# Kernel optimization log

Hardware: AMD Instinct MI355X
Metric: run time of the kernel (lower is better)

## Reference

```python
import jax, jax.numpy as jnp
import numpy as np

E, H, FF = 1024, 16, 4096
HD = E // H
B, S = 4, 2048


def _ln(x, g, b, eps=1e-5):
    m = jnp.mean(x, axis=-1, keepdims=True)
    v = jnp.mean((x - m) ** 2, axis=-1, keepdims=True)
    return (x - m) / jnp.sqrt(v + eps) * g + b


def setup_inputs() -> dict:
    k = jax.random.key(0)
    ks = jax.random.split(k, 12)
    sd = 0.02
    return {
        "value": jax.random.normal(ks[0], (B, S, E), jnp.float32),
        "key": jax.random.normal(ks[1], (B, S, E), jnp.float32),
        "query": jax.random.normal(ks[2], (B, S, E), jnp.float32),
        "mask": jnp.ones((B, 1, 1, S), jnp.int32),
        "Wv": sd * jax.random.normal(ks[3], (E, E), jnp.float32),
        "Wk": sd * jax.random.normal(ks[4], (E, E), jnp.float32),
        "Wq": sd * jax.random.normal(ks[5], (E, E), jnp.float32),
        "Wo": sd * jax.random.normal(ks[6], (E, E), jnp.float32),
        "bo": jnp.zeros((E,), jnp.float32),
        "ln1_g": jnp.ones((E,), jnp.float32), "ln1_b": jnp.zeros((E,), jnp.float32),
        "ln2_g": jnp.ones((E,), jnp.float32), "ln2_b": jnp.zeros((E,), jnp.float32),
        "lnf_g": jnp.ones((E,), jnp.float32), "lnf_b": jnp.zeros((E,), jnp.float32),
        "W1": sd * jax.random.normal(ks[7], (E, FF), jnp.float32),
        "b1": jnp.zeros((FF,), jnp.float32),
        "W2": sd * jax.random.normal(ks[8], (FF, E), jnp.float32),
        "b2": jnp.zeros((E,), jnp.float32),
    }


def reference(value, key, query, mask, Wv, Wk, Wq, Wo, bo,
              ln1_g, ln1_b, ln2_g, ln2_b, lnf_g, lnf_b, W1, b1, W2, b2):
    N, Sq, Em = query.shape
    # pre-norms (value & key share prenorm2 params, as in the torch module)
    v = _ln(value, ln2_g, ln2_b)
    k = _ln(key, ln2_g, ln2_b)
    q = _ln(query, ln1_g, ln1_b)
    # QKV projections (no bias), split heads
    V = (v @ Wv).reshape(N, v.shape[1], H, HD)
    K = (k @ Wk).reshape(N, k.shape[1], H, HD)
    Q = (q @ Wq).reshape(N, Sq, H, HD)
    energy = jnp.einsum("nqhd,nkhd->nhqk", Q, K)  # [N,H,Sq,Sk]
    energy = jnp.where(mask == 0, jnp.float32(-1e20), energy)
    attn = jax.nn.softmax(energy / jnp.float32(HD ** 0.5), axis=-1)
    out = jnp.einsum("nhqk,nkhd->nqhd", attn, V).reshape(N, Sq, Em)
    out = out @ Wo + bo
    x = out + q  # residual (drop_path is identity in eval)
    f = _ln(x, lnf_g, lnf_b) @ W1 + b1
    f = jax.nn.gelu(f, approximate=False) @ W2 + b2
    return f + x
```

## Files before the change

### kernel.cpp

```cpp
#include <hip/hip_runtime.h>
#include <hip/hip_bf16.h>
#include <math.h>

typedef __bf16 bf16x8 __attribute__((ext_vector_type(8)));
typedef __bf16 bf16x4 __attribute__((ext_vector_type(4)));
typedef float f32x4 __attribute__((ext_vector_type(4)));
typedef float f32x2 __attribute__((ext_vector_type(2)));
typedef short s16x4 __attribute__((ext_vector_type(4)));

#define AS1 __attribute__((address_space(1)))
#define AS3 __attribute__((address_space(3)))

__device__ __forceinline__ void gll16(const __bf16* g, __bf16* l) {
    __builtin_amdgcn_global_load_lds((const AS1 unsigned int*)g,
                                     (AS3 unsigned int*)l, 16, 0, 0);
}

#if __has_builtin(__builtin_amdgcn_exp2f)
#define EXP2(x) __builtin_amdgcn_exp2f(x)
#else
#define EXP2(x) __expf((x) * 0.69314718055994530942f)
#endif

__device__ __forceinline__ f32x4 mfma16x16(bf16x4 a, bf16x4 b, f32x4 c) {
#if __has_builtin(__builtin_amdgcn_mfma_f32_16x16x16bf16_1k)
    union { bf16x4 h; s16x4 s; } ua, ub;
    ua.h = a; ub.h = b;
    return __builtin_amdgcn_mfma_f32_16x16x16bf16_1k(ua.s, ub.s, c, 0, 0, 0);
#else
    f32x4 d = c;
    asm volatile("v_mfma_f32_16x16x16_bf16 %0, %1, %2, %0"
                 : "+v"(d) : "v"(a), "v"(b));
    return d;
#endif
}

__global__ __launch_bounds__(256) void transpose_all(
    const float* __restrict__ Wq, const float* __restrict__ Wk,
    const float* __restrict__ Wv, const float* __restrict__ Wo,
    const float* __restrict__ W1, const float* __restrict__ W2,
    __bf16* __restrict__ Wqt, __bf16* __restrict__ Wkt,
    __bf16* __restrict__ Wvt, __bf16* __restrict__ Wot,
    __bf16* __restrict__ W1t, __bf16* __restrict__ W2t) {
    int g = blockIdx.x;
    const float* W; __bf16* Wt; int K, N, kt, nt;
    if (g < 4096) {
        int mi = g >> 10, loc = g & 1023;
        K = 1024; N = 1024; kt = loc >> 5; nt = loc & 31;
        W  = mi == 0 ? Wq  : mi == 1 ? Wk  : mi == 2 ? Wv  : Wo;
        Wt = mi == 0 ? Wqt : mi == 1 ? Wkt : mi == 2 ? Wvt : Wot;
    } else if (g < 8192) {
        int loc = g - 4096; W = W1; Wt = W1t;
        K = 1024; N = 4096; kt = loc >> 7; nt = loc & 127;
    } else {
        int loc = g - 8192; W = W2; Wt = W2t;
        K = 4096; N = 1024; kt = loc >> 5; nt = loc & 31;
    }
    int k0 = kt * 32, n0 = nt * 32;
    __shared__ float tile[32][33];
    int tx = threadIdx.x & 31, ty = threadIdx.x >> 5;
    #pragma unroll
    for (int j = ty; j < 32; j += 8)
        tile[j][tx] = W[(size_t)(k0 + j) * N + n0 + tx];
    __syncthreads();
    #pragma unroll
    for (int j = ty; j < 32; j += 8)
        Wt[(size_t)(n0 + j) * K + k0 + tx] = (__bf16)tile[tx][j];
}

__global__ __launch_bounds__(256) void ln3_kernel(
    const float* __restrict__ q, const float* __restrict__ k,
    const float* __restrict__ v,
    const float* __restrict__ g1, const float* __restrict__ b1,
    const float* __restrict__ g2, const float* __restrict__ b2,
    float* __restrict__ qln, __bf16* __restrict__ qbf,
    __bf16* __restrict__ kbf, __bf16* __restrict__ vbf) {
    const int E = 1024;
    int which = blockIdx.y;
    const float* x = which == 0 ? q : which == 1 ? k : v;
    const float* g = which == 0 ? g1 : g2;
    const float* bb = which == 0 ? b1 : b2;
    float* o32 = which == 0 ? qln : nullptr;
    __bf16* obf = which == 0 ? qbf : which == 1 ? kbf : vbf;

    size_t row = blockIdx.x;
    int t = threadIdx.x;
    float4 val = ((const float4*)(x + row * E))[t];
    float s  = val.x + val.y + val.z + val.w;
    float s2 = val.x * val.x + val.y * val.y + val.z * val.z + val.w * val.w;
    #pragma unroll
    for (int off = 32; off >= 1; off >>= 1) {
        s  += __shfl_down(s, off);
        s2 += __shfl_down(s2, off);
    }
    __shared__ float red[2][4];
    int wid = t >> 6, lane = t & 63;
    if (lane == 0) { red[0][wid] = s; red[1][wid] = s2; }
    __syncthreads();
    if (t == 0) {
        float S1 = red[0][0] + red[0][1] + red[0][2] + red[0][3];
        float S2 = red[1][0] + red[1][1] + red[1][2] + red[1][3];
        float mean = S1 / E;
        float var  = S2 / E - mean * mean;
        red[0][0] = mean;
        red[1][0] = 1.0f / sqrtf(var + 1e-5f);
    }
    __syncthreads();
    float mean = red[0][0], rstd = red[1][0];
    float4 gv = ((const float4*)g)[t];
    float4 bv = ((const float4*)bb)[t];
    float y0 = (val.x - mean) * rstd * gv.x + bv.x;
    float y1 = (val.y - mean) * rstd * gv.y + bv.y;
    float y2 = (val.z - mean) * rstd * gv.z + bv.z;
    float y3 = (val.w - mean) * rstd * gv.w + bv.w;
    if (o32) ((float4*)(o32 + row * E))[t] = make_float4(y0, y1, y2, y3);
    bf16x4 o;
    o[0] = (__bf16)y0; o[1] = (__bf16)y1; o[2] = (__bf16)y2; o[3] = (__bf16)y3;
    ((bf16x4*)(obf + row * E))[t] = o;
}

__global__ __launch_bounds__(256) void ln_kernel(const float* __restrict__ x,
                                                 const float* __restrict__ g,
                                                 const float* __restrict__ bb,
                                                 __bf16* __restrict__ outbf) {
    const int E = 1024;
    size_t row = blockIdx.x;
    int t = threadIdx.x;
    float4 v = ((const float4*)(x + row * E))[t];
    float s  = v.x + v.y + v.z + v.w;
    float s2 = v.x * v.x + v.y * v.y + v.z * v.z + v.w * v.w;
    #pragma unroll
    for (int off = 32; off >= 1; off >>= 1) {
        s  += __shfl_down(s, off);
        s2 += __shfl_down(s2, off);
    }
    __shared__ float red[2][4];
    int wid = t >> 6, lane = t & 63;
    if (lane == 0) { red[0][wid] = s; red[1][wid] = s2; }
    __syncthreads();
    if (t == 0) {
        float S1 = red[0][0] + red[0][1] + red[0][2] + red[0][3];
        float S2 = red[1][0] + red[1][1] + red[1][2] + red[1][3];
        float mean = S1 / E;
        float var  = S2 / E - mean * mean;
        red[0][0] = mean;
        red[1][0] = 1.0f / sqrtf(var + 1e-5f);
    }
    __syncthreads();
    float mean = red[0][0], rstd = red[1][0];
    float4 gv = ((const float4*)g)[t];
    float4 bv = ((const float4*)bb)[t];
    bf16x4 o;
    o[0] = (__bf16)((v.x - mean) * rstd * gv.x + bv.x);
    o[1] = (__bf16)((v.y - mean) * rstd * gv.y + bv.y);
    o[2] = (__bf16)((v.z - mean) * rstd * gv.z + bv.z);
    o[3] = (__bf16)((v.w - mean) * rstd * gv.w + bv.w);
    ((bf16x4*)(outbf + row * E))[t] = o;
}

template <int EPI>
__global__ __launch_bounds__(256) void gemm128(const __bf16* __restrict__ A,
                                               const __bf16* __restrict__ A2,
                                               const __bf16* __restrict__ Bt,
                                               const __bf16* __restrict__ Bt2,
                                               const float* __restrict__ bias,
                                               const float* __restrict__ resid,
                                               void* __restrict__ Cout,
                                               int M, int N, int K,
                                               int splitN, float scale) {
    __shared__ __bf16 As[128 * 64];
    __shared__ __bf16 Bs[128 * 64];
    int tid  = threadIdx.x;
    int lane = tid & 63, wid = tid >> 6;
    int quad = lane >> 4, l15 = lane & 15;
    int waveM = wid >> 1, waveN = wid & 1;

    int GX = N >> 7;
    int id = blockIdx.x;
    int x8 = id & 7, t = id >> 3;
    size_t rowBase = (size_t)((t / GX) * 8 + x8) * 128;
    size_t colBase = (size_t)(t % GX) * 128;

    const __bf16* Ap = A; const __bf16* Bp = Bt;
    size_t colLoc = colBase;
    float sc = scale;
    if ((int)colBase >= splitN) { Ap = A2; Bp = Bt2; colLoc = colBase - splitN; sc = 1.0f; }

    int lrow8  = lane >> 3;
    int lchunk = (lane & 7) ^ lrow8;
    const __bf16* Ag0 = Ap + (rowBase + wid * 32 + lrow8) * (size_t)K + lchunk * 8;
    const __bf16* Bg0 = Bp + (colLoc  + wid * 32 + lrow8) * (size_t)K + lchunk * 8;
    __bf16* AsB = &As[(wid * 32) * 64];
    __bf16* BsB = &Bs[(wid * 32) * 64];

    f32x4 acc[4][4] = {};
    int swz = l15 & 7;

    for (int kb = 0; kb < K; kb += 64) {
        __syncthreads();
        #pragma unroll
        for (int i = 0; i < 4; i++) {
            gll16(Ag0 + (size_t)i * 8 * K + kb, AsB + i * 512);
            gll16(Bg0 + (size_t)i * 8 * K + kb, BsB + i * 512);
        }
        __syncthreads();
        #pragma unroll
        for (int ks = 0; ks < 2; ks++) {
            int p = ((ks * 4 + quad) ^ swz) * 8;
            bf16x8 af[4], bfr[4];
            #pragma unroll
            for (int mi = 0; mi < 4; mi++)
                af[mi] = *(const bf16x8*)&As[(waveM * 64 + mi * 16 + l15) * 64 + p];
            #pragma unroll
            for (int ni = 0; ni < 4; ni++)
                bfr[ni] = *(const bf16x8*)&Bs[(waveN * 64 + ni * 16 + l15) * 64 + p];
            #pragma unroll
            for (int mi = 0; mi < 4; mi++)
                #pragma unroll
                for (int ni = 0; ni < 4; ni++)
                    acc[mi][ni] = __builtin_amdgcn_mfma_f32_16x16x32_bf16(
                        bfr[ni], af[mi], acc[mi][ni], 0, 0, 0);
        }
    }

    #pragma unroll
    for (int mi = 0; mi < 4; mi++)
    #pragma unroll
    for (int ni = 0; ni < 4; ni++) {
        size_t row = rowBase + waveM * 64 + mi * 16 + l15;
        size_t col = colBase + waveN * 64 + ni * 16 + quad * 4;
        f32x4 v = acc[mi][ni];
        if (EPI == 1) {
            float4 b4 = *(const float4*)&bias[col];
            float4 r4 = *(const float4*)&resid[row * N + col];
            float4 o;
            o.x = v[0] + b4.x + r4.x; o.y = v[1] + b4.y + r4.y;
            o.z = v[2] + b4.z + r4.z; o.w = v[3] + b4.w + r4.w;
            *(float4*)&((float*)Cout)[row * N + col] = o;
        } else if (EPI == 2) {
            float4 b4 = *(const float4*)&bias[col];
            bf16x4 pk;
            #pragma unroll
            for (int r = 0; r < 4; r++) {
                float t2 = v[r] + ((const float*)&b4)[r];
                pk[r] = (__bf16)(0.5f * t2 * (1.0f + erff(t2 * 0.70710678118654752f)));
            }
            *(bf16x4*)&((__bf16*)Cout)[row * N + col] = pk;
        } else {
            bf16x4 pk;
            #pragma unroll
            for (int r = 0; r < 4; r++) pk[r] = (__bf16)(v[r] * sc);
            *(bf16x4*)&((__bf16*)Cout)[row * N + col] = pk;
        }
    }
}

template <int EPI>
__global__ __launch_bounds__(512, 2) void gemm256(const __bf16* __restrict__ A,
                                                  const __bf16* __restrict__ A2,
                                                  const __bf16* __restrict__ Bt,
                                                  const __bf16* __restrict__ Bt2,
                                                  const float* __restrict__ bias,
                                                  const float* __restrict__ resid,
                                                  void* __restrict__ Cout,
                                                  int M, int N, int K,
                                                  int splitN, float scale) {
    __shared__ __bf16 As[2][256 * 64];
    __shared__ __bf16 Bs[2][256 * 64];
    int tid  = threadIdx.x;
    int lane = tid & 63, wid = tid >> 6;
    int quad = lane >> 4, l15 = lane & 15;
    int waveM = wid >> 2, waveN = wid & 3;

    int GX = N >> 8;
    int id = blockIdx.x;
    int x8 = id & 7, tt = id >> 3;
    size_t rowBase = (size_t)((tt / GX) * 8 + x8) * 256;
    size_t colBase = (size_t)(tt % GX) * 256;

    const __bf16* Ap = A; const __bf16* Bp = Bt;
    size_t colLoc = colBase;
    float sc = scale;
    if ((int)colBase >= splitN) { Ap = A2; Bp = Bt2; colLoc = colBase - splitN; sc = 1.0f; }

    int lrow8  = lane >> 3;
    int lchunk = (lane & 7) ^ lrow8;
    const __bf16* Ag0 = Ap + (rowBase + wid * 32 + lrow8) * (size_t)K + lchunk * 8;
    const __bf16* Bg0 = Bp + (colLoc  + wid * 32 + lrow8) * (size_t)K + lchunk * 8;
    int ldsB = (wid * 32) * 64;

    f32x4 acc[8][4] = {};
    int swz = l15 & 7;
    int nsteps = K >> 6;

    #pragma unroll
    for (int i = 0; i < 4; i++) {
        gll16(Ag0 + (size_t)i * 8 * K, &As[0][ldsB + i * 512]);
        gll16(Bg0 + (size_t)i * 8 * K, &Bs[0][ldsB + i * 512]);
    }
    __syncthreads();

    for (int t = 0; t < nsteps; t++) {
        int cur = t & 1;
        const __bf16* Asb = &As[cur][0];
        const __bf16* Bsb = &Bs[cur][0];
        __bf16* Asn = &As[cur ^ 1][0];
        __bf16* Bsn = &Bs[cur ^ 1][0];
        bool pre = (t + 1 < nsteps);
        size_t kb = (size_t)(t + 1) << 6;

        bf16x8 af[4], bfr[4];
        int p0 = (quad ^ swz) * 8;
        int p1 = ((4 + quad) ^ swz) * 8;

        #pragma unroll
        for (int ni = 0; ni < 4; ni++)
            bfr[ni] = *(const bf16x8*)&Bsb[(waveN * 64 + ni * 16 + l15) * 64 + p0];
        #pragma unroll
        for (int mi = 0; mi < 4; mi++)
            af[mi] = *(const bf16x8*)&Asb[(waveM * 128 + mi * 16 + l15) * 64 + p0];
        if (pre) {
            #pragma unroll
            for (int i = 0; i < 4; i++)
                gll16(Ag0 + (size_t)i * 8 * K + kb, &Asn[ldsB + i * 512]);
        }
        __builtin_amdgcn_s_barrier();
        __builtin_amdgcn_s_setprio(1);
        #pragma unroll
        for (int mi = 0; mi < 4; mi++)
            #pragma unroll
            for (int ni = 0; ni < 4; ni++)
                acc[mi][ni] = __builtin_amdgcn_mfma_f32_16x16x32_bf16(
                    bfr[ni], af[mi], acc[mi][ni], 0, 0, 0);
        __builtin_amdgcn_s_setprio(0);
        __builtin_amdgcn_s_barrier();

        #pragma unroll
        for (int mi = 0; mi < 4; mi++)
            af[mi] = *(const bf16x8*)&Asb[(waveM * 128 + (mi + 4) * 16 + l15) * 64 + p0];
        if (pre) {
            #pragma unroll
            for (int i = 0; i < 4; i++)
                gll16(Bg0 + (size_t)i * 8 * K + kb, &Bsn[ldsB + i * 512]);
        }
        __builtin_amdgcn_s_barrier();
        __builtin_amdgcn_s_setprio(1);
        #pragma unroll
        for (int mi = 0; mi < 4; mi++)
            #pragma unroll
            for (int ni = 0; ni < 4; ni++)
                acc[mi + 4][ni] = __builtin_amdgcn_mfma_f32_16x16x32_bf16(
                    bfr[ni], af[mi], acc[mi + 4][ni], 0, 0, 0);
        __builtin_amdgcn_s_setprio(0);
        __builtin_amdgcn_s_barrier();

        #pragma unroll
        for (int ni = 0; ni < 4; ni++)
            bfr[ni] = *(const bf16x8*)&Bsb[(waveN * 64 + ni * 16 + l15) * 64 + p1];
        #pragma unroll
        for (int mi = 0; mi < 4; mi++)
            af[mi] = *(const bf16x8*)&Asb[(waveM * 128 + mi * 16 + l15) * 64 + p1];
        __builtin_amdgcn_s_barrier();
        __builtin_amdgcn_s_setprio(1);
        #pragma unroll
        for (int mi = 0; mi < 4; mi++)
            #pragma unroll
            for (int ni = 0; ni < 4; ni++)
                acc[mi][ni] = __builtin_amdgcn_mfma_f32_16x16x32_bf16(
                    bfr[ni], af[mi], acc[mi][ni], 0, 0, 0);
        __builtin_amdgcn_s_setprio(0);
        __builtin_amdgcn_s_barrier();

        #pragma unroll
        for (int mi = 0; mi < 4; mi++)
            af[mi] = *(const bf16x8*)&Asb[(waveM * 128 + (mi + 4) * 16 + l15) * 64 + p1];
        __builtin_amdgcn_s_setprio(1);
        #pragma unroll
        for (int mi = 0; mi < 4; mi++)
            #pragma unroll
            for (int ni = 0; ni < 4; ni++)
                acc[mi + 4][ni] = __builtin_amdgcn_mfma_f32_16x16x32_bf16(
                    bfr[ni], af[mi], acc[mi + 4][ni], 0, 0, 0);
        __builtin_amdgcn_s_setprio(0);
        __syncthreads();
    }

    #pragma unroll
    for (int mi = 0; mi < 8; mi++)
    #pragma unroll
    for (int ni = 0; ni < 4; ni++) {
        size_t row = rowBase + waveM * 128 + mi * 16 + l15;
        size_t col = colBase + waveN * 64 + ni * 16 + quad * 4;
        f32x4 v = acc[mi][ni];
        if (EPI == 1) {
            float4 b4 = *(const float4*)&bias[col];
            float4 r4 = *(const float4*)&resid[row * N + col];
            float4 o;
            o.x = v[0] + b4.x + r4.x; o.y = v[1] + b4.y + r4.y;
            o.z = v[2] + b4.z + r4.z; o.w = v[3] + b4.w + r4.w;
            *(float4*)&((float*)Cout)[row * N + col] = o;
        } else if (EPI == 2) {
            float4 b4 = *(const float4*)&bias[col];
            bf16x4 pk;
            #pragma unroll
            for (int r = 0; r < 4; r++) {
                float t2 = v[r] + ((const float*)&b4)[r];
                pk[r] = (__bf16)(0.5f * t2 * (1.0f + erff(t2 * 0.70710678118654752f)));
            }
            *(bf16x4*)&((__bf16*)Cout)[row * N + col] = pk;
        } else {
            bf16x4 pk;
            #pragma unroll
            for (int r = 0; r < 4; r++) pk[r] = (__bf16)(v[r] * sc);
            *(bf16x4*)&((__bf16*)Cout)[row * N + col] = pk;
        }
    }
}

__global__ __launch_bounds__(256) void gemmV(const __bf16* __restrict__ A,
                                             const __bf16* __restrict__ Bt,
                                             __bf16* __restrict__ Cout,
                                             int M, int N, int K) {
    __shared__ __bf16 As[128 * 64];
    __shared__ __bf16 Bs[128 * 64];
    int tid  = threadIdx.x;
    int lane = tid & 63, wid = tid >> 6;
    int quad = lane >> 4, l15 = lane & 15;
    int waveM = wid >> 1, waveN = wid & 1;

    int GX = N >> 7;
    int id = blockIdx.x;
    int x8 = id & 7, t = id >> 3;
    size_t rowBase = (size_t)((t / GX) * 8 + x8) * 128;
    size_t colBase = (size_t)(t % GX) * 128;

    int lrow8  = lane >> 3;
    int lchunk = (lane & 7) ^ lrow8;
    const __bf16* Ag0 = A  + (rowBase + wid * 32 + lrow8) * (size_t)K + lchunk * 8;
    const __bf16* Bg0 = Bt + (colBase + wid * 32 + lrow8) * (size_t)K + lchunk * 8;
    __bf16* AsB = &As[(wid * 32) * 64];
    __bf16* BsB = &Bs[(wid * 32) * 64];

    f32x4 acc[4][4] = {};
    int swz = l15 & 7;

    for (int kb = 0; kb < K; kb += 64) {
        __syncthreads();
        #pragma unroll
        for (int i = 0; i < 4; i++) {
            gll16(Ag0 + (size_t)i * 8 * K + kb, AsB + i * 512);
            gll16(Bg0 + (size_t)i * 8 * K + kb, BsB + i * 512);
        }
        __syncthreads();
        #pragma unroll
        for (int ks = 0; ks < 2; ks++) {
            int p = ((ks * 4 + quad) ^ swz) * 8;
            bf16x8 af[4], bfr[4];
            #pragma unroll
            for (int mi = 0; mi < 4; mi++)
                af[mi] = *(const bf16x8*)&As[(waveM * 64 + mi * 16 + l15) * 64 + p];
            #pragma unroll
            for (int ni = 0; ni < 4; ni++)
                bfr[ni] = *(const bf16x8*)&Bs[(waveN * 64 + ni * 16 + l15) * 64 + p];
            #pragma unroll
            for (int mi = 0; mi < 4; mi++)
                #pragma unroll
                for (int ni = 0; ni < 4; ni++)
                    acc[mi][ni] = __builtin_amdgcn_mfma_f32_16x16x32_bf16(
                        af[mi], bfr[ni], acc[mi][ni], 0, 0, 0);
        }
    }

    #pragma unroll
    for (int mi = 0; mi < 4; mi++)
    #pragma unroll
    for (int ni = 0; ni < 4; ni++) {
        size_t col = colBase + waveN * 64 + ni * 16 + l15;
        size_t m0  = rowBase + waveM * 64 + mi * 16 + quad * 4;
        bf16x4 pk;
        #pragma unroll
        for (int r = 0; r < 4; r++) pk[r] = (__bf16)acc[mi][ni][r];
        *(bf16x4*)&Cout[col * M + m0] = pk;
    }
}

__global__ __launch_bounds__(512, 4) void attn_kernel(const __bf16* __restrict__ QK,
                                                      const __bf16* __restrict__ Vt,
                                                      const int* __restrict__ mask,
                                                      __bf16* __restrict__ Out) {
    const int S = 2048, E = 1024, E2 = 2048, M = 8192;
    int qt = blockIdx.x, bh = blockIdx.y;
    int b = bh >> 4, h = bh & 15;
    int q0 = qt * 256;
    int tid = threadIdx.x, lane = tid & 63, wid = tid >> 6;
    int quad = lane >> 4, l15 = lane & 15;

    __shared__ __bf16 Ks[2][4096];
    __shared__ __bf16 Vs[2][4096];

    bf16x8 aq[2][2];
    #pragma unroll
    for (int g = 0; g < 2; g++)
    #pragma unroll
    for (int hh = 0; hh < 2; hh++) {
        size_t row = (size_t)(b * S + q0 + wid * 32 + g * 16 + l15);
        aq[g][hh] = *(const bf16x8*)(QK + row * E2 + h * 64 + hh * 32 + quad * 8);
    }

    int lrow8  = lane >> 3;
    int lchunk = (lane & 7) ^ lrow8;
    const __bf16* Kg0 = QK + (size_t)(b * S + wid * 8 + lrow8) * E2 + 1024 + h * 64 + lchunk * 8;

    int rv = tid >> 3, cv = tid & 7;
    const __bf16* Vg0 = Vt + (size_t)(h * 64 + rv) * M + b * S + cv * 8;
    int c0   = ((cv & 1) << 2) + (cv >> 2);
    int lowb = (cv >> 1) & 1;
    int sv   = rv & 7;
    int wo0  = rv * 64 + ((c0 ^ sv) << 3) + (lowb << 2);
    int wo1  = rv * 64 + (((c0 + 2) ^ sv) << 3) + (lowb << 2);

    int swz = l15 & 7;

    f32x4 accO[2][4] = {};
    f32x2 acc2[2] = {};

    bf16x8 vreg = *(const bf16x8*)(Vg0);
    gll16(Kg0, &Ks[0][wid * 512]);
    *(bf16x4*)&Vs[0][wo0] = __builtin_shufflevector(vreg, vreg, 0, 1, 2, 3);
    *(bf16x4*)&Vs[0][wo1] = __builtin_shufflevector(vreg, vreg, 4, 5, 6, 7);
    __syncthreads();

    for (int kt = 0; kt < S / 64; kt++) {
        int k0 = kt * 64;
        int buf = kt & 1;
        if (kt + 1 < S / 64) {
            vreg = *(const bf16x8*)(Vg0 + k0 + 64);
            gll16(Kg0 + (size_t)(k0 + 64) * E2, &Ks[buf ^ 1][wid * 512]);
        }
        const __bf16* Ksb = &Ks[buf][0];
        const __bf16* Vsb = &Vs[buf][0];

        bf16x4 pb[2][4];
        #pragma unroll
        for (int nt = 0; nt < 4; nt++) {
            bf16x8 a0 = *(const bf16x8*)&Ksb[(nt * 16 + l15) * 64 + ((quad) ^ swz) * 8];
            bf16x8 a1 = *(const bf16x8*)&Ksb[(nt * 16 + l15) * 64 + ((4 + quad) ^ swz) * 8];
            int4 mz = *(const int4*)&mask[b * S + k0 + nt * 16 + quad * 4];
            #pragma unroll
            for (int g = 0; g < 2; g++) {
                f32x4 a = {};
                a = __builtin_amdgcn_mfma_f32_16x16x32_bf16(a0, aq[g][0], a, 0, 0, 0);
                a = __builtin_amdgcn_mfma_f32_16x16x32_bf16(a1, aq[g][1], a, 0, 0, 0);
                float p0 = mz.x ? EXP2(a[0]) : 0.f;
                float p1 = mz.y ? EXP2(a[1]) : 0.f;
                float p2 = mz.z ? EXP2(a[2]) : 0.f;
                float p3 = mz.w ? EXP2(a[3]) : 0.f;
                f32x2 t01; t01[0] = p0; t01[1] = p1;
                f32x2 t23; t23[0] = p2; t23[1] = p3;
                acc2[g] += t01 + t23;
                bf16x4 pk;
                pk[0] = (__bf16)p0; pk[1] = (__bf16)p1;
                pk[2] = (__bf16)p2; pk[3] = (__bf16)p3;
                pb[g][nt] = pk;
            }
        }

        #pragma unroll
        for (int dt = 0; dt < 4; dt++) {
            const __bf16* vrow = &Vsb[(dt * 16 + l15) * 64];
            bf16x8 vv0 = *(const bf16x8*)&vrow[((quad * 2 + 0) ^ swz) * 8];
            bf16x8 vv1 = *(const bf16x8*)&vrow[((quad * 2 + 1) ^ swz) * 8];
            bf16x4 h00 = __builtin_shufflevector(vv0, vv0, 0, 1, 2, 3);
            bf16x4 h01 = __builtin_shufflevector(vv0, vv0, 4, 5, 6, 7);
            bf16x4 h10 = __builtin_shufflevector(vv1, vv1, 0, 1, 2, 3);
            bf16x4 h11 = __builtin_shufflevector(vv1, vv1, 4, 5, 6, 7);
            #pragma unroll
            for (int g = 0; g < 2; g++) {
                accO[g][dt] = mfma16x16(h00, pb[g][0], accO[g][dt]);
                accO[g][dt] = mfma16x16(h01, pb[g][1], accO[g][dt]);
                accO[g][dt] = mfma16x16(h10, pb[g][2], accO[g][dt]);
                accO[g][dt] = mfma16x16(h11, pb[g][3], accO[g][dt]);
            }
        }

        if (kt + 1 < S / 64) {
            *(bf16x4*)&Vs[buf ^ 1][wo0] = __builtin_shufflevector(vreg, vreg, 0, 1, 2, 3);
            *(bf16x4*)&Vs[buf ^ 1][wo1] = __builtin_shufflevector(vreg, vreg, 4, 5, 6, 7);
        }
        __syncthreads();
    }

    #pragma unroll
    for (int g = 0; g < 2; g++) {
        float l = acc2[g][0] + acc2[g][1];
        l += __shfl_xor(l, 16, 64);
        l += __shfl_xor(l, 32, 64);
        float inv = 1.0f / l;
        #pragma unroll
        for (int dt = 0; dt < 4; dt++) {
            size_t row = (size_t)(b * S + q0 + wid * 32 + g * 16 + l15);
            bf16x4 pk;
            #pragma unroll
            for (int r = 0; r < 4; r++) pk[r] = (__bf16)(accO[g][dt][r] * inv);
            *(bf16x4*)&Out[row * E + h * 64 + dt * 16 + quad * 4] = pk;
        }
    }
}

extern "C" void kernel_launch(void* const* d_in, const int* in_sizes, int n_in,
                              void* d_out, int out_size, void* d_ws, size_t ws_size,
                              hipStream_t stream) {
    const int Bb = 4, S = 2048, E = 1024, FF = 4096;
    const int M = Bb * S;

    const float* value = (const float*)d_in[0];
    const float* key   = (const float*)d_in[1];
    const float* query = (const float*)d_in[2];
    const int*   mask  = (const int*)d_in[3];
    const float* Wv    = (const float*)d_in[4];
    const float* Wk    = (const float*)d_in[5];
    const float* Wq    = (const float*)d_in[6];
    const float* Wo    = (const float*)d_in[7];
    const float* bo    = (const float*)d_in[8];
    const float* ln1_g = (const float*)d_in[9];
    const float* ln1_b = (const float*)d_in[10];
    const float* ln2_g = (const float*)d_in[11];
    const float* ln2_b = (const float*)d_in[12];
    const float* lnf_g = (const float*)d_in[13];
    const float* lnf_b = (const float*)d_in[14];
    const float* W1    = (const float*)d_in[15];
    const float* b1    = (const float*)d_in[16];
    const float* W2    = (const float*)d_in[17];
    const float* b2    = (const float*)d_in[18];

    char* ws = (char*)d_ws;
    const size_t MB = 1024 * 1024;
    __bf16* Wqt = (__bf16*)(ws + 0 * MB);
    __bf16* Wkt = (__bf16*)(ws + 2 * MB);
    __bf16* Wvt = (__bf16*)(ws + 4 * MB);
    __bf16* Wot = (__bf16*)(ws + 6 * MB);
    __bf16* W1t = (__bf16*)(ws + 8 * MB);
    __bf16* W2t = (__bf16*)(ws + 16 * MB);
    __bf16* q_bf = (__bf16*)(ws + 24 * MB);
    __bf16* k_bf = (__bf16*)(ws + 40 * MB);
    __bf16* v_bf = (__bf16*)(ws + 56 * MB);
    __bf16* QKb  = (__bf16*)(ws + 72 * MB);
    __bf16* Vtg  = (__bf16*)(ws + 104 * MB);
    __bf16* attn = q_bf;
    __bf16* x_ln = k_bf;
    __bf16* h1   = v_bf;
    float*  qln  = (float*)(ws + 120 * MB);
    float*  x32  = (float*)(ws + 152 * MB);

    transpose_all<<<12288, 256, 0, stream>>>(Wq, Wk, Wv, Wo, W1, W2,
                                             Wqt, Wkt, Wvt, Wot, W1t, W2t);

    ln3_kernel<<<dim3(M, 3), 256, 0, stream>>>(query, key, value,
                                               ln1_g, ln1_b, ln2_g, ln2_b,
                                               qln, q_bf, k_bf, v_bf);

    gemm256<0><<<256, 512, 0, stream>>>(
        q_bf, k_bf, Wqt, Wkt, nullptr, nullptr, QKb, M, 2 * E, E, E,
        0.125f * 1.44269504088896f);

    gemmV<<<8 * 64, 256, 0, stream>>>(v_bf, Wvt, Vtg, M, E, E);

    attn_kernel<<<dim3(S / 256, Bb * 16), 512, 0, stream>>>(QKb, Vtg, mask, attn);

    gemm128<1><<<8 * 64, 256, 0, stream>>>(
        attn, attn, Wot, Wot, bo, qln, x32, M, E, E, E, 1.0f);

    ln_kernel<<<M, 256, 0, stream>>>(x32, lnf_g, lnf_b, x_ln);

    gemm256<2><<<512, 512, 0, stream>>>(
        x_ln, x_ln, W1t, W1t, b1, nullptr, h1, M, FF, E, FF, 1.0f);
    gemm128<1><<<8 * 64, 256, 0, stream>>>(
        h1, h1, W2t, W2t, b2, x32, (float*)d_out, M, E, FF, E, 1.0f);
}
```

Measured before the change: 623.9 us.

## Restructure GEMM pipelines with finer-grained staged prefetch and a triple-buffered 256x128 kernel

The 256x256 GEMM's double-buffered loop is rewritten into a 2-step unrolled schedule. Global-to-LDS loads are split into half-tile stages interleaved with MFMA phases and gated by explicit vmcnt waits, so loads stay in flight across barriers. The gemm128 kernel used for the Wo and W2 projections is replaced by a new 256x128-tile, 512-thread kernel with a 3-stage LDS ring buffer and prefetch two steps ahead. This aims to hide memory latency and raise MFMA utilization, at the cost of more LDS per block and manual waitcnt ordering that must stay correct.

```diff
diff --git a/kernel.cpp b/kernel.cpp
--- a/kernel.cpp
+++ b/kernel.cpp
@@ -15,6 +15,8 @@
     __builtin_amdgcn_global_load_lds((const AS1 unsigned int*)g,
                                      (AS3 unsigned int*)l, 16, 0, 0);
 }
+
+#define VMCNT(n) asm volatile("s_waitcnt vmcnt(" #n ")" ::: "memory")
 
 #if __has_builtin(__builtin_amdgcn_exp2f)
 #define EXP2(x) __builtin_amdgcn_exp2f(x)
@@ -159,103 +161,6 @@
 }
 
 template <int EPI>
-__global__ __launch_bounds__(256) void gemm128(const __bf16* __restrict__ A,
-                                               const __bf16* __restrict__ A2,
-                                               const __bf16* __restrict__ Bt,
-                                               const __bf16* __restrict__ Bt2,
-                                               const float* __restrict__ bias,
-                                               const float* __restrict__ resid,
-                                               void* __restrict__ Cout,
-                                               int M, int N, int K,
-                                               int splitN, float scale) {
-    __shared__ __bf16 As[128 * 64];
-    __shared__ __bf16 Bs[128 * 64];
-    int tid  = threadIdx.x;
-    int lane = tid & 63, wid = tid >> 6;
-    int quad = lane >> 4, l15 = lane & 15;
-    int waveM = wid >> 1, waveN = wid & 1;
-
-    int GX = N >> 7;
-    int id = blockIdx.x;
-    int x8 = id & 7, t = id >> 3;
-    size_t rowBase = (size_t)((t / GX) * 8 + x8) * 128;
-    size_t colBase = (size_t)(t % GX) * 128;
-
-    const __bf16* Ap = A; const __bf16* Bp = Bt;
-    size_t colLoc = colBase;
-    float sc = scale;
-    if ((int)colBase >= splitN) { Ap = A2; Bp = Bt2; colLoc = colBase - splitN; sc = 1.0f; }
-
-    int lrow8  = lane >> 3;
-    int lchunk = (lane & 7) ^ lrow8;
-    const __bf16* Ag0 = Ap + (rowBase + wid * 32 + lrow8) * (size_t)K + lchunk * 8;
-    const __bf16* Bg0 = Bp + (colLoc  + wid * 32 + lrow8) * (size_t)K + lchunk * 8;
-    __bf16* AsB = &As[(wid * 32) * 64];
-    __bf16* BsB = &Bs[(wid * 32) * 64];
-
-    f32x4 acc[4][4] = {};
-    int swz = l15 & 7;
-
-    for (int kb = 0; kb < K; kb += 64) {
-        __syncthreads();
-        #pragma unroll
-        for (int i = 0; i < 4; i++) {
-            gll16(Ag0 + (size_t)i * 8 * K + kb, AsB + i * 512);
-            gll16(Bg0 + (size_t)i * 8 * K + kb, BsB + i * 512);
-        }
-        __syncthreads();
-        #pragma unroll
-        for (int ks = 0; ks < 2; ks++) {
-            int p = ((ks * 4 + quad) ^ swz) * 8;
-            bf16x8 af[4], bfr[4];
-            #pragma unroll
-            for (int mi = 0; mi < 4; mi++)
-                af[mi] = *(const bf16x8*)&As[(waveM * 64 + mi * 16 + l15) * 64 + p];
-            #pragma unroll
-            for (int ni = 0; ni < 4; ni++)
-                bfr[ni] = *(const bf16x8*)&Bs[(waveN * 64 + ni * 16 + l15) * 64 + p];
-            #pragma unroll
-            for (int mi = 0; mi < 4; mi++)
-                #pragma unroll
-                for (int ni = 0; ni < 4; ni++)
-                    acc[mi][ni] = __builtin_amdgcn_mfma_f32_16x16x32_bf16(
-                        bfr[ni], af[mi], acc[mi][ni], 0, 0, 0);
-        }
-    }
-
-    #pragma unroll
-    for (int mi = 0; mi < 4; mi++)
-    #pragma unroll
-    for (int ni = 0; ni < 4; ni++) {
-        size_t row = rowBase + waveM * 64 + mi * 16 + l15;
-        size_t col = colBase + waveN * 64 + ni * 16 + quad * 4;
-        f32x4 v = acc[mi][ni];
-        if (EPI == 1) {
-            float4 b4 = *(const float4*)&bias[col];
-            float4 r4 = *(const float4*)&resid[row * N + col];
-            float4 o;
-            o.x = v[0] + b4.x + r4.x; o.y = v[1] + b4.y + r4.y;
-            o.z = v[2] + b4.z + r4.z; o.w = v[3] + b4.w + r4.w;
-            *(float4*)&((float*)Cout)[row * N + col] = o;
-        } else if (EPI == 2) {
-            float4 b4 = *(const float4*)&bias[col];
-            bf16x4 pk;
-            #pragma unroll
-            for (int r = 0; r < 4; r++) {
-                float t2 = v[r] + ((const float*)&b4)[r];
-                pk[r] = (__bf16)(0.5f * t2 * (1.0f + erff(t2 * 0.70710678118654752f)));
-            }
-            *(bf16x4*)&((__bf16*)Cout)[row * N + col] = pk;
-        } else {
-            bf16x4 pk;
-            #pragma unroll
-            for (int r = 0; r < 4; r++) pk[r] = (__bf16)(v[r] * sc);
-            *(bf16x4*)&((__bf16*)Cout)[row * N + col] = pk;
-        }
-    }
-}
-
-template <int EPI>
 __global__ __launch_bounds__(512, 2) void gemm256(const __bf16* __restrict__ A,
                                                   const __bf16* __restrict__ A2,
                                                   const __bf16* __restrict__ Bt,
@@ -285,105 +190,80 @@
 
     int lrow8  = lane >> 3;
     int lchunk = (lane & 7) ^ lrow8;
-    const __bf16* Ag0 = Ap + (rowBase + wid * 32 + lrow8) * (size_t)K + lchunk * 8;
-    const __bf16* Bg0 = Bp + (colLoc  + wid * 32 + lrow8) * (size_t)K + lchunk * 8;
-    int ldsB = (wid * 32) * 64;
+    const __bf16* AgH = Ap + (rowBase + wid * 8 + lrow8) * (size_t)K + lchunk * 8;
+    const __bf16* BgH = Bp + (colLoc  + wid * 8 + lrow8) * (size_t)K + lchunk * 8;
+
+#define STAGE_A256(buf, h, kt) do { \
+    gll16(AgH + (size_t)((h) * 128) * K + (size_t)(kt) * 64,      &As[buf][((h) * 128 + wid * 8) * 64]); \
+    gll16(AgH + (size_t)((h) * 128 + 64) * K + (size_t)(kt) * 64, &As[buf][((h) * 128 + wid * 8 + 64) * 64]); \
+} while (0)
+#define STAGE_B256(buf, h, kt) do { \
+    gll16(BgH + (size_t)((h) * 128) * K + (size_t)(kt) * 64,      &Bs[buf][((h) * 128 + wid * 8) * 64]); \
+    gll16(BgH + (size_t)((h) * 128 + 64) * K + (size_t)(kt) * 64, &Bs[buf][((h) * 128 + wid * 8 + 64) * 64]); \
+} while (0)
 
     f32x4 acc[8][4] = {};
     int swz = l15 & 7;
     int nsteps = K >> 6;
 
-    #pragma unroll
-    for (int i = 0; i < 4; i++) {
-        gll16(Ag0 + (size_t)i * 8 * K, &As[0][ldsB + i * 512]);
-        gll16(Bg0 + (size_t)i * 8 * K, &Bs[0][ldsB + i * 512]);
-    }
-    __syncthreads();
-
-    for (int t = 0; t < nsteps; t++) {
-        int cur = t & 1;
-        const __bf16* Asb = &As[cur][0];
-        const __bf16* Bsb = &Bs[cur][0];
-        __bf16* Asn = &As[cur ^ 1][0];
-        __bf16* Bsn = &Bs[cur ^ 1][0];
-        bool pre = (t + 1 < nsteps);
-        size_t kb = (size_t)(t + 1) << 6;
-
-        bf16x8 af[4], bfr[4];
-        int p0 = (quad ^ swz) * 8;
-        int p1 = ((4 + quad) ^ swz) * 8;
-
-        #pragma unroll
-        for (int ni = 0; ni < 4; ni++)
-            bfr[ni] = *(const bf16x8*)&Bsb[(waveN * 64 + ni * 16 + l15) * 64 + p0];
-        #pragma unroll
-        for (int mi = 0; mi < 4; mi++)
-            af[mi] = *(const bf16x8*)&Asb[(waveM * 128 + mi * 16 + l15) * 64 + p0];
-        if (pre) {
-            #pragma unroll
-            for (int i = 0; i < 4; i++)
-                gll16(Ag0 + (size_t)i * 8 * K + kb, &Asn[ldsB + i * 512]);
-        }
-        __builtin_amdgcn_s_barrier();
-        __builtin_amdgcn_s_setprio(1);
-        #pragma unroll
-        for (int mi = 0; mi < 4; mi++)
-            #pragma unroll
-            for (int ni = 0; ni < 4; ni++)
-                acc[mi][ni] = __builtin_amdgcn_mfma_f32_16x16x32_bf16(
-                    bfr[ni], af[mi], acc[mi][ni], 0, 0, 0);
-        __builtin_amdgcn_s_setprio(0);
-        __builtin_amdgcn_s_barrier();
-
-        #pragma unroll
-        for (int mi = 0; mi < 4; mi++)
-            af[mi] = *(const bf16x8*)&Asb[(waveM * 128 + (mi + 4) * 16 + l15) * 64 + p0];
-        if (pre) {
-            #pragma unroll
-            for (int i = 0; i < 4; i++)
-                gll16(Bg0 + (size_t)i * 8 * K + kb, &Bsn[ldsB + i * 512]);
-        }
-        __builtin_amdgcn_s_barrier();
-        __builtin_amdgcn_s_setprio(1);
-        #pragma unroll
-        for (int mi = 0; mi < 4; mi++)
-            #pragma unroll
-            for (int ni = 0; ni < 4; ni++)
-                acc[mi + 4][ni] = __builtin_amdgcn_mfma_f32_16x16x32_bf16(
-                    bfr[ni], af[mi], acc[mi + 4][ni], 0, 0, 0);
-        __builtin_amdgcn_s_setprio(0);
-        __builtin_amdgcn_s_barrier();
-
-        #pragma unroll
-        for (int ni = 0; ni < 4; ni++)
-            bfr[ni] = *(const bf16x8*)&Bsb[(waveN * 64 + ni * 16 + l15) * 64 + p1];
-        #pragma unroll
-        for (int mi = 0; mi < 4; mi++)
-            af[mi] = *(const bf16x8*)&Asb[(waveM * 128 + mi * 16 + l15) * 64 + p1];
-        __builtin_amdgcn_s_barrier();
-        __builtin_amdgcn_s_setprio(1);
-        #pragma unroll
-        for (int mi = 0; mi < 4; mi++)
-            #pragma unroll
-            for (int ni = 0; ni < 4; ni++)
-                acc[mi][ni] = __builtin_amdgcn_mfma_f32_16x16x32_bf16(
-                    bfr[ni], af[mi], acc[mi][ni], 0, 0, 0);
-        __builtin_amdgcn_s_setprio(0);
-        __builtin_amdgcn_s_barrier();
-
-        #pragma unroll
-        for (int mi = 0; mi < 4; mi++)
-            af[mi] = *(const bf16x8*)&Asb[(waveM * 128 + (mi + 4) * 16 + l15) * 64 + p1];
-        __builtin_amdgcn_s_setprio(1);
-        #pragma unroll
-        for (int mi = 0; mi < 4; mi++)
-            #pragma unroll
-            for (int ni = 0; ni < 4; ni++)
-                acc[mi + 4][ni] = __builtin_amdgcn_mfma_f32_16x16x32_bf16(
-                    bfr[ni], af[mi], acc[mi + 4][ni], 0, 0, 0);
-        __builtin_amdgcn_s_setprio(0);
-        __syncthreads();
-    }
+    STAGE_B256(0, 0, 0); STAGE_B256(0, 1, 0);
+    STAGE_A256(0, 0, 0); STAGE_A256(0, 1, 0);
+    STAGE_B256(1, 0, 1);
+    VMCNT(2);
+    __builtin_amdgcn_s_barrier();
+
+    bf16x8 af[4], bfr[4];
+    int p0 = (quad ^ swz) * 8;
+    int p1 = ((4 + quad) ^ swz) * 8;
+
+#define RD_B(buf, p) { _Pragma("unroll") \
+    for (int ni = 0; ni < 4; ni++) \
+        bfr[ni] = *(const bf16x8*)&Bs[buf][(waveN * 64 + ni * 16 + l15) * 64 + (p)]; }
+#define RD_A(buf, mo, p) { _Pragma("unroll") \
+    for (int mi = 0; mi < 4; mi++) \
+        af[mi] = *(const bf16x8*)&As[buf][(waveM * 128 + ((mo) + mi) * 16 + l15) * 64 + (p)]; }
+#define DO_MFMA(ao) { __builtin_amdgcn_s_barrier(); __builtin_amdgcn_s_setprio(1); \
+    _Pragma("unroll") for (int mi = 0; mi < 4; mi++) \
+    _Pragma("unroll") for (int ni = 0; ni < 4; ni++) \
+        acc[(ao) + mi][ni] = __builtin_amdgcn_mfma_f32_16x16x32_bf16( \
+            bfr[ni], af[mi], acc[(ao) + mi][ni], 0, 0, 0); \
+    __builtin_amdgcn_s_setprio(0); __builtin_amdgcn_s_barrier(); }
+
+    for (int T = 0; T < nsteps; T += 2) {
+        int S2 = T + 2 < nsteps ? T + 2 : nsteps - 1;
+        int S3 = T + 3 < nsteps ? T + 3 : nsteps - 1;
+        RD_B(0, p0); RD_A(0, 0, p0);
+        STAGE_B256(1, 1, T + 1);
+        DO_MFMA(0);
+        RD_A(0, 4, p0);
+        STAGE_A256(1, 0, T + 1);
+        DO_MFMA(4);
+        RD_B(0, p1); RD_A(0, 0, p1);
+        STAGE_A256(1, 1, T + 1);
+        DO_MFMA(0);
+        RD_A(0, 4, p1);
+        STAGE_B256(0, 0, S2);
+        VMCNT(2);
+        DO_MFMA(4);
+        RD_B(1, p0); RD_A(1, 0, p0);
+        STAGE_B256(0, 1, S2);
+        DO_MFMA(0);
+        RD_A(1, 4, p0);
+        STAGE_A256(0, 0, S2);
+        DO_MFMA(4);
+        RD_B(1, p1); RD_A(1, 0, p1);
+        STAGE_A256(0, 1, S2);
+        DO_MFMA(0);
+        RD_A(1, 4, p1);
+        STAGE_B256(1, 0, S3);
+        VMCNT(2);
+        DO_MFMA(4);
+    }
+#undef RD_B
+#undef RD_A
+#undef DO_MFMA
+#undef STAGE_A256
+#undef STAGE_B256
 
     #pragma unroll
     for (int mi = 0; mi < 8; mi++)
@@ -412,6 +292,135 @@
             bf16x4 pk;
             #pragma unroll
             for (int r = 0; r < 4; r++) pk[r] = (__bf16)(v[r] * sc);
+            *(bf16x4*)&((__bf16*)Cout)[row * N + col] = pk;
+        }
+    }
+}
+
+template <int EPI>
+__global__ __launch_bounds__(512, 2) void gemm256x128(const __bf16* __restrict__ A,
+                                                      const __bf16* __restrict__ Bt,
+                                                      const float* __restrict__ bias,
+                                                      const float* __restrict__ resid,
+                                                      void* __restrict__ Cout,
+                                                      int M, int N, int K,
+                                                      float scale) {
+    __shared__ __bf16 As[3][256 * 64];
+    __shared__ __bf16 Bs[3][128 * 64];
+    int tid  = threadIdx.x;
+    int lane = tid & 63, wid = tid >> 6;
+    int quad = lane >> 4, l15 = lane & 15;
+    int waveM = wid >> 1, waveN = wid & 1;
+
+    int GX = N >> 7;
+    int id = blockIdx.x;
+    int x8 = id & 7, tt = id >> 3;
+    size_t rowBase = (size_t)((tt / GX) * 8 + x8) * 256;
+    size_t colBase = (size_t)(tt % GX) * 128;
+
+    int lrow8  = lane >> 3;
+    int lchunk = (lane & 7) ^ lrow8;
+    const __bf16* Ag0 = A  + (rowBase + wid * 32 + lrow8) * (size_t)K + lchunk * 8;
+    const __bf16* Bg0 = Bt + (colBase + wid * 16 + lrow8) * (size_t)K + lchunk * 8;
+    int ldsA = (wid * 32) * 64;
+    int ldsB = (wid * 16) * 64;
+
+#define STAGE_A4(buf, kt) { _Pragma("unroll") \
+    for (int i = 0; i < 4; i++) \
+        gll16(Ag0 + (size_t)i * 8 * K + (size_t)(kt) * 64, &As[buf][ldsA + i * 512]); }
+#define STAGE_B2(buf, kt) { _Pragma("unroll") \
+    for (int i = 0; i < 2; i++) \
+        gll16(Bg0 + (size_t)i * 8 * K + (size_t)(kt) * 64, &Bs[buf][ldsB + i * 512]); }
+
+    f32x4 acc[4][4] = {};
+    int swz = l15 & 7;
+    int nsteps = K >> 6;
+
+    STAGE_A4(0, 0); STAGE_B2(0, 0);
+    STAGE_A4(1, 1); STAGE_B2(1, 1);
+    VMCNT(6);
+    __builtin_amdgcn_s_barrier();
+
+    bf16x8 af[4], bfr[4];
+    int p0 = (quad ^ swz) * 8;
+    int p1 = ((4 + quad) ^ swz) * 8;
+
+    int cb = 0;
+    for (int T = 0; T < nsteps; T++) {
+        int nb = cb + 2; if (nb >= 3) nb -= 3;
+        int S = T + 2 < nsteps ? T + 2 : nsteps - 1;
+        const __bf16* Asb = &As[cb][0];
+        const __bf16* Bsb = &Bs[cb][0];
+
+        #pragma unroll
+        for (int ni = 0; ni < 4; ni++)
+            bfr[ni] = *(const bf16x8*)&Bsb[(waveN * 64 + ni * 16 + l15) * 64 + p0];
+        #pragma unroll
+        for (int mi = 0; mi < 4; mi++)
+            af[mi] = *(const bf16x8*)&Asb[(waveM * 64 + mi * 16 + l15) * 64 + p0];
+        STAGE_A4(nb, S);
+        __builtin_amdgcn_s_barrier();
+        __builtin_amdgcn_s_setprio(1);
+        #pragma unroll
+        for (int mi = 0; mi < 4; mi++)
+            #pragma unroll
+            for (int ni = 0; ni < 4; ni++)
+                acc[mi][ni] = __builtin_amdgcn_mfma_f32_16x16x32_bf16(
+                    bfr[ni], af[mi], acc[mi][ni], 0, 0, 0);
+        __builtin_amdgcn_s_setprio(0);
+        __builtin_amdgcn_s_barrier();
+
+        #pragma unroll
+        for (int ni = 0; ni < 4; ni++)
+            bfr[ni] = *(const bf16x8*)&Bsb[(waveN * 64 + ni * 16 + l15) * 64 + p1];
+        #pragma unroll
+        for (int mi = 0; mi < 4; mi++)
+            af[mi] = *(const bf16x8*)&Asb[(waveM * 64 + mi * 16 + l15) * 64 + p1];
+        STAGE_B2(nb, S);
+        VMCNT(6);
+        __builtin_amdgcn_s_barrier();
+        __builtin_amdgcn_s_setprio(1);
+        #pragma unroll
+        for (int mi = 0; mi < 4; mi++)
+            #pragma unroll
+            for (int ni = 0; ni < 4; ni++)
+                acc[mi][ni] = __builtin_amdgcn_mfma_f32_16x16x32_bf16(
+                    bfr[ni], af[mi], acc[mi][ni], 0, 0, 0);
+        __builtin_amdgcn_s_setprio(0);
+        __builtin_amdgcn_s_barrier();
+
+        cb = cb + 1 == 3 ? 0 : cb + 1;
+    }
+#undef STAGE_A4
+#undef STAGE_B2
+
+    #pragma unroll
+    for (int mi = 0; mi < 4; mi++)
+    #pragma unroll
+    for (int ni = 0; ni < 4; ni++) {
+        size_t row = rowBase + waveM * 64 + mi * 16 + l15;
+        size_t col = colBase + waveN * 64 + ni * 16 + quad * 4;
+        f32x4 v = acc[mi][ni];
+        if (EPI == 1) {
+            float4 b4 = *(const float4*)&bias[col];
+            float4 r4 = *(const float4*)&resid[row * N + col];
+            float4 o;
+            o.x = v[0] + b4.x + r4.x; o.y = v[1] + b4.y + r4.y;
+            o.z = v[2] + b4.z + r4.z; o.w = v[3] + b4.w + r4.w;
+            *(float4*)&((float*)Cout)[row * N + col] = o;
+        } else if (EPI == 2) {
+            float4 b4 = *(const float4*)&bias[col];
+            bf16x4 pk;
+            #pragma unroll
+            for (int r = 0; r < 4; r++) {
+                float t2 = v[r] + ((const float*)&b4)[r];
+                pk[r] = (__bf16)(0.5f * t2 * (1.0f + erff(t2 * 0.70710678118654752f)));
+            }
+            *(bf16x4*)&((__bf16*)Cout)[row * N + col] = pk;
+        } else {
+            bf16x4 pk;
+            #pragma unroll
+            for (int r = 0; r < 4; r++) pk[r] = (__bf16)(v[r] * scale);
             *(bf16x4*)&((__bf16*)Cout)[row * N + col] = pk;
         }
     }
@@ -667,13 +676,13 @@
 
     attn_kernel<<<dim3(S / 256, Bb * 16), 512, 0, stream>>>(QKb, Vtg, mask, attn);
 
-    gemm128<1><<<8 * 64, 256, 0, stream>>>(
-        attn, attn, Wot, Wot, bo, qln, x32, M, E, E, E, 1.0f);
+    gemm256x128<1><<<256, 512, 0, stream>>>(
+        attn, Wot, bo, qln, x32, M, E, E, 1.0f);
 
     ln_kernel<<<M, 256, 0, stream>>>(x32, lnf_g, lnf_b, x_ln);
 
     gemm256<2><<<512, 512, 0, stream>>>(
         x_ln, x_ln, W1t, W1t, b1, nullptr, h1, M, FF, E, FF, 1.0f);
-    gemm128<1><<<8 * 64, 256, 0, stream>>>(
-        h1, h1, W2t, W2t, b2, x32, (float*)d_out, M, E, FF, E, 1.0f);
-}
+    gemm256x128<1><<<256, 512, 0, stream>>>(
+        h1, W2t, b2, x32, (float*)d_out, M, E, FF, 1.0f);
+}
```

Measured after the change: 628.4 us. About the same (+0.7%).
